# Kernel tuning notes

Measured on AMD Instinct MI355X. Metric: run time of the kernel, lower is better.

Reference implementation:

```python
import jax, jax.numpy as jnp
import numpy as np

B, H, T = 32, 80, 1600
C1, C2 = 32, 32
K, S, P = 3, 2, 1  # kernel, stride, padding on both dims


def setup_inputs() -> dict:
    key = jax.random.key(0)
    k1, k2, k3, k4, k5, k6 = jax.random.split(key, 6)
    inputs = jax.random.normal(k1, (B, 1, H, T), dtype=jnp.float32)
    seq_lengths = jax.random.randint(k2, (B,), 1, T + 1).astype(jnp.int32)
    W1 = jax.random.normal(k3, (C1, 1, K, K), dtype=jnp.float32) * 0.1
    b1 = jax.random.normal(k4, (C1,), dtype=jnp.float32) * 0.1
    W2 = jax.random.normal(k5, (C2, C1, K, K), dtype=jnp.float32) * 0.05
    b2 = jax.random.normal(k6, (C2,), dtype=jnp.float32) * 0.1
    return {"inputs": inputs, "seq_lengths": seq_lengths,
            "W1": W1, "b1": b1, "W2": W2, "b2": b2}


def _conv(x, W, b):
    y = jax.lax.conv_general_dilated(
        x, W, window_strides=(S, S), padding=((P, P), (P, P)),
        dimension_numbers=("NCHW", "OIHW", "NCHW"))
    return y + b[None, :, None, None]


def _new_lengths(L):
    # floor((L + 2p - d*(k-1) - 1)/s) + 1, matching _get_sequence_lengths
    return (L + 2 * P - (K - 1) - 1) // S + 1


def _mask_time(x, L):
    # zero positions t >= L[b] along the last (time) axis
    t = jnp.arange(x.shape[3])
    valid = (t[None, :] < L[:, None]).astype(x.dtype)  # [B, Tout]
    return x * valid[:, None, None, :]


def reference(inputs, seq_lengths, W1, b1, W2, b2):
    # conv1 + mask
    x = _conv(inputs, W1, b1)
    L = _new_lengths(seq_lengths)
    x = _mask_time(x, L)
    # relu + mask (lengths unchanged)
    x = _mask_time(jax.nn.relu(x), L)
    # conv2 + mask
    x = _conv(x, W2, b2)
    L = _new_lengths(L)
    x = _mask_time(x, L)
    # relu + mask
    x = _mask_time(jax.nn.relu(x), L)
    return x, L
```

## Files before the change

kernel.cpp:

```cpp
#include <hip/hip_runtime.h>
#include <hip/hip_bf16.h>

#define B_    32
#define H_IN  80
#define T_IN  1600
#define C1_   32
#define H1_   40
#define T1_   800
#define C2_   32
#define H2_   20
#define T2_   400

#define TH2   2
#define TT2   32
#define NH1   5
#define NT1   65
#define NIDX  33
#define RROWS 11
#define RCW   68
#define NX4   (RROWS * 34)

#define NPOS   (NH1 * NT1)
#define NCHUNK 11

#define WS_W2FRAGS 1152
#define WS_W1OFF   1152
#define WS_TOTAL   1216
#define OUTN  (B_ * C2_ * H2_ * T2_)

typedef unsigned int uint32;
typedef __attribute__((ext_vector_type(8)))  short short8;
typedef __attribute__((ext_vector_type(4)))  float f32x4;
typedef __attribute__((ext_vector_type(16))) float f32x16;
typedef __attribute__((ext_vector_type(2)))  uint32 u32x2;
typedef __attribute__((ext_vector_type(4)))  uint32 u32x4;

__device__ __forceinline__ unsigned short f2bf(float x) {
    __hip_bfloat16 h = __float2bfloat16(x);
    return __builtin_bit_cast(unsigned short, h);
}

__device__ __forceinline__ int x1off(int h1r, int t1r, int g) {
    int idx = t1r >> 1;
    int par = t1r & 1;
    return ((par * (NH1 * NIDX) + h1r * NIDX + idx) << 6) + (((g ^ idx) & 3) << 4);
}

__global__ void wprep(const float* __restrict__ W2, const float* __restrict__ W1,
                      const float* __restrict__ b1, unsigned short* __restrict__ ws) {
    int i = blockIdx.x * 256 + threadIdx.x;
    if (i < WS_W2FRAGS) {
        int mt   = i / 576;
        int rem  = i - mt * 576;
        int tap  = rem >> 6;
        int lane = rem & 63;
        int lg   = lane >> 4;
        int l15  = lane & 15;
        int c2   = mt * 16 + l15;
        short8 f;
#pragma unroll
        for (int j = 0; j < 8; ++j)
            f[j] = (short)f2bf(W2[((c2 * C1_) + lg * 8 + j) * 9 + tap]);
        *((short8*)ws + i) = f;
    } else if (i < WS_TOTAL) {
        int lane = i - WS_W1OFF;
        int c1 = lane & 31;
        int kb = (lane >> 5) * 8;
        short8 f;
#pragma unroll
        for (int j = 0; j < 8; ++j) {
            int k = kb + j;
            float v = (k < 9) ? W1[c1 * 9 + k] : (k == 9 ? b1[c1] : 0.0f);
            f[j] = (short)f2bf(v);
        }
        *((short8*)ws + i) = f;
    }
}

__global__ __launch_bounds__(256, 6) void fused_conv(
    const float* __restrict__ in, const int* __restrict__ seq,
    const float* __restrict__ b2,
    const unsigned short* __restrict__ ws,
    float* __restrict__ out)
{
    __shared__ __align__(16) char   x1mem[2 * NH1 * NIDX * 64];
    __shared__ __align__(16) uint32 raw32[RROWS * RCW];

    const int tid  = threadIdx.x;
    const int lane = tid & 63;
    const int wv   = tid >> 6;
    const int l15  = lane & 15;
    const int lg   = lane >> 4;
    const int hi   = lane >> 5;
    const int n32  = lane & 31;
    const int b      = blockIdx.z;
    const int h2base = blockIdx.y * TH2;
    const int t2base = blockIdx.x * TT2;

    const int L  = seq[b];
    const int L1 = ((L  - 1) >> 1) + 1;
    const int L2 = ((L1 - 1) >> 1) + 1;

    if (blockIdx.x == 0 && blockIdx.y == 0 && tid == 0)
        out[OUTN + b] = (float)L2;

    if (t2base >= L2) {
        const f32x4 z4 = (f32x4){0.f, 0.f, 0.f, 0.f};
#pragma unroll
        for (int k = 0; k < 2; ++k) {
            int i = tid + k * 256;
            int row = i >> 3, q = i & 7;
            int c2 = row >> 1, r = row & 1;
            int t2g = t2base + 4 * q;
            if (t2g < T2_)
                __builtin_nontemporal_store(z4,
                    (f32x4*)(out + ((b * C2_ + c2) * H2_ + h2base + r) * T2_ + t2g));
        }
        return;
    }

    const int row0 = 4 * h2base - 3;
    const int tA   = 4 * t2base - 4;
    const float* inb = in + b * (H_IN * T_IN);
#pragma unroll
    for (int k = 0; k < 2; ++k) {
        int it = tid + k * 256;
        if (it < NX4) {
            int row = it / 34;
            int j   = it - row * 34;
            int h = row0 + row;
            int t = tA + 4 * j;
            bool okq = (h >= 0) & (h < H_IN) & (t >= 0) & (t < T_IN);
            int basec = okq ? (h * T_IN + t) : 0;
            f32x4 v = *(const f32x4*)(inb + basec);
            float f0 = okq ? v[0] : 0.0f;
            float f1 = okq ? v[1] : 0.0f;
            float f2 = okq ? v[2] : 0.0f;
            float f3 = okq ? v[3] : 0.0f;
            u32x2 dw;
            dw.x = (uint32)f2bf(f0) | ((uint32)f2bf(f1) << 16);
            dw.y = (uint32)f2bf(f2) | ((uint32)f2bf(f3) << 16);
            *(u32x2*)(raw32 + row * RCW + 2 * j) = dw;
        }
    }

    const short8 w1f = *((const short8*)ws + WS_W1OFF + lane);
    const int mt    = wv & 1;
    const int strip = wv >> 1;
    short8 afr[9];
#pragma unroll
    for (int tap = 0; tap < 9; ++tap)
        afr[tap] = *((const short8*)ws + (mt * 9 + tap) * 64 + lane);
    float b2r[4];
#pragma unroll
    for (int j = 0; j < 4; ++j) b2r[j] = b2[mt * 16 + lg * 4 + j];

    __syncthreads();

    const int h1base = 2 * h2base - 1;
    const int t1base = 2 * t2base - 1;
    for (int c = wv; c < NCHUNK; c += 4) {
        int p  = c * 32 + n32;
        int pc = p < NPOS ? p : NPOS - 1;
        int h1r = pc / NT1;
        int t1r = pc - h1r * NT1;

        const uint32* rp = raw32 + (2 * h1r) * RCW + t1r;
        uint32 a0 = rp[0],          b0v = rp[1];
        uint32 a1 = rp[RCW],        b1v = rp[RCW + 1];
        uint32 a2 = rp[2 * RCW],    b2v = rp[2 * RCW + 1];

        uint32 w0l = (a0 >> 16) | (b0v << 16);
        uint32 w1l = (b0v >> 16) | (a1 & 0xffff0000u);
        uint32 w2l = b1v;
        uint32 w3l = (a2 >> 16) | (b2v << 16);
        uint32 w0h = (b2v >> 16) | 0x3f800000u;

        uint32 fw0 = hi ? w0h : w0l;
        uint32 fw1 = hi ? 0u  : w1l;
        uint32 fw2 = hi ? 0u  : w2l;
        uint32 fw3 = hi ? 0u  : w3l;
        short8 bfrag = __builtin_bit_cast(short8, (u32x4){fw0, fw1, fw2, fw3});

        f32x16 acc = {};
        acc = __builtin_amdgcn_mfma_f32_32x32x16_bf16(w1f, bfrag, acc, 0, 0, 0);

        int h1 = h1base + h1r;
        int t1 = t1base + t1r;
        bool okp = (h1 >= 0) && (t1 >= 0) && (t1 < L1);
        if (p < NPOS) {
#pragma unroll
            for (int g = 0; g < 4; ++g) {
                float v0 = okp ? fmaxf(acc[4 * g + 0], 0.0f) : 0.0f;
                float v1 = okp ? fmaxf(acc[4 * g + 1], 0.0f) : 0.0f;
                float v2 = okp ? fmaxf(acc[4 * g + 2], 0.0f) : 0.0f;
                float v3 = okp ? fmaxf(acc[4 * g + 3], 0.0f) : 0.0f;
                u32x2 dw;
                dw.x = (uint32)f2bf(v0) | ((uint32)f2bf(v1) << 16);
                dw.y = (uint32)f2bf(v2) | ((uint32)f2bf(v3) << 16);
                *(u32x2*)(x1mem + x1off(h1r, t1r, g) + hi * 8) = dw;
            }
        }
    }

    __syncthreads();

    f32x4 acc2[TH2];
#pragma unroll
    for (int r = 0; r < TH2; ++r) acc2[r] = (f32x4){0.f, 0.f, 0.f, 0.f};

#pragma unroll
    for (int tap = 0; tap < 9; ++tap) {
        const int kh = tap / 3;
        const int kt = tap % 3;
        const int t1r = 2 * (strip * 16 + l15) + kt;
#pragma unroll
        for (int r = 0; r < TH2; ++r) {
            short8 bx = *(const short8*)(x1mem + x1off(2 * r + kh, t1r, lg));
            acc2[r] = __builtin_amdgcn_mfma_f32_16x16x32_bf16(afr[tap], bx, acc2[r], 0, 0, 0);
        }
    }

    {
        const int t2 = t2base + strip * 16 + l15;
        const bool vm = (t2 < L2);
        if (t2 < T2_) {
            float* outb = out + ((b * C2_) * H2_ + h2base) * T2_ + t2;
#pragma unroll
            for (int r = 0; r < TH2; ++r) {
#pragma unroll
                for (int j = 0; j < 4; ++j) {
                    int c2 = mt * 16 + lg * 4 + j;
                    float v = acc2[r][j] + b2r[j];
                    v = vm ? fmaxf(v, 0.0f) : 0.0f;
                    __builtin_nontemporal_store(v, outb + (c2 * H2_ + r) * T2_);
                }
            }
        }
    }
}

extern "C" void kernel_launch(void* const* d_in, const int* in_sizes, int n_in,
                              void* d_out, int out_size, void* d_ws, size_t ws_size,
                              hipStream_t stream) {
    const float* in  = (const float*)d_in[0];
    const int*   seq = (const int*)d_in[1];
    const float* W1  = (const float*)d_in[2];
    const float* b1  = (const float*)d_in[3];
    const float* W2  = (const float*)d_in[4];
    const float* b2  = (const float*)d_in[5];
    float* out = (float*)d_out;
    unsigned short* ws = (unsigned short*)d_ws;

    wprep<<<dim3((WS_TOTAL + 255) / 256), dim3(256), 0, stream>>>(W2, W1, b1, ws);

    dim3 grid((T2_ + TT2 - 1) / TT2, H2_ / TH2, B_);
    fused_conv<<<grid, dim3(256), 0, stream>>>(in, seq, b2, ws, out);
}
```

Measured before the change: 22.27 us.

## Make fused conv persistent with atomic tile scheduler and register-prefetched input

```diff
diff --git a/kernel.cpp b/kernel.cpp
--- a/kernel.cpp
+++ b/kernel.cpp
@@ -23,9 +23,15 @@
 #define NPOS   (NH1 * NT1)
 #define NCHUNK 11
 
+#define NT2I   13
+#define NH2I   10
+#define NTILES (NT2I * NH2I * B_)
+#define NBLK   1536
+
 #define WS_W2FRAGS 1152
 #define WS_W1OFF   1152
 #define WS_TOTAL   1216
+#define CTR_OFF    (WS_TOTAL * 16)
 #define OUTN  (B_ * C2_ * H2_ * T2_)
 
 typedef unsigned int uint32;
@@ -49,6 +55,7 @@
 __global__ void wprep(const float* __restrict__ W2, const float* __restrict__ W1,
                       const float* __restrict__ b1, unsigned short* __restrict__ ws) {
     int i = blockIdx.x * 256 + threadIdx.x;
+    if (i == 0) *(uint32*)((char*)ws + CTR_OFF) = 0u;
     if (i < WS_W2FRAGS) {
         int mt   = i / 576;
         int rem  = i - mt * 576;
@@ -77,14 +84,41 @@
     }
 }
 
+__device__ __forceinline__ void stage_to_regs(const float* __restrict__ inb, int tid,
+                                              int h2base, int t2base, u32x2 dw[2]) {
+    const int row0 = 4 * h2base - 3;
+    const int tA   = 4 * t2base - 4;
+#pragma unroll
+    for (int k = 0; k < 2; ++k) {
+        int it = tid + k * 256;
+        u32x2 d = (u32x2){0u, 0u};
+        if (it < NX4) {
+            int row = it / 34;
+            int j   = it - row * 34;
+            int h = row0 + row;
+            int t = tA + 4 * j;
+            bool okq = (h >= 0) & (h < H_IN) & (t >= 0) & (t < T_IN);
+            f32x4 v = *(const f32x4*)(inb + (okq ? h * T_IN + t : 0));
+            float f0 = okq ? v[0] : 0.0f;
+            float f1 = okq ? v[1] : 0.0f;
+            float f2 = okq ? v[2] : 0.0f;
+            float f3 = okq ? v[3] : 0.0f;
+            d.x = (uint32)f2bf(f0) | ((uint32)f2bf(f1) << 16);
+            d.y = (uint32)f2bf(f2) | ((uint32)f2bf(f3) << 16);
+        }
+        dw[k] = d;
+    }
+}
+
 __global__ __launch_bounds__(256, 6) void fused_conv(
     const float* __restrict__ in, const int* __restrict__ seq,
     const float* __restrict__ b2,
-    const unsigned short* __restrict__ ws,
+    unsigned short* __restrict__ ws,
     float* __restrict__ out)
 {
     __shared__ __align__(16) char   x1mem[2 * NH1 * NIDX * 64];
     __shared__ __align__(16) uint32 raw32[RROWS * RCW];
+    __shared__ int s_tile[2];
 
     const int tid  = threadIdx.x;
     const int lane = tid & 63;
@@ -93,56 +127,8 @@
     const int lg   = lane >> 4;
     const int hi   = lane >> 5;
     const int n32  = lane & 31;
-    const int b      = blockIdx.z;
-    const int h2base = blockIdx.y * TH2;
-    const int t2base = blockIdx.x * TT2;
-
-    const int L  = seq[b];
-    const int L1 = ((L  - 1) >> 1) + 1;
-    const int L2 = ((L1 - 1) >> 1) + 1;
-
-    if (blockIdx.x == 0 && blockIdx.y == 0 && tid == 0)
-        out[OUTN + b] = (float)L2;
-
-    if (t2base >= L2) {
-        const f32x4 z4 = (f32x4){0.f, 0.f, 0.f, 0.f};
-#pragma unroll
-        for (int k = 0; k < 2; ++k) {
-            int i = tid + k * 256;
-            int row = i >> 3, q = i & 7;
-            int c2 = row >> 1, r = row & 1;
-            int t2g = t2base + 4 * q;
-            if (t2g < T2_)
-                __builtin_nontemporal_store(z4,
-                    (f32x4*)(out + ((b * C2_ + c2) * H2_ + h2base + r) * T2_ + t2g));
-        }
-        return;
-    }
-
-    const int row0 = 4 * h2base - 3;
-    const int tA   = 4 * t2base - 4;
-    const float* inb = in + b * (H_IN * T_IN);
-#pragma unroll
-    for (int k = 0; k < 2; ++k) {
-        int it = tid + k * 256;
-        if (it < NX4) {
-            int row = it / 34;
-            int j   = it - row * 34;
-            int h = row0 + row;
-            int t = tA + 4 * j;
-            bool okq = (h >= 0) & (h < H_IN) & (t >= 0) & (t < T_IN);
-            int basec = okq ? (h * T_IN + t) : 0;
-            f32x4 v = *(const f32x4*)(inb + basec);
-            float f0 = okq ? v[0] : 0.0f;
-            float f1 = okq ? v[1] : 0.0f;
-            float f2 = okq ? v[2] : 0.0f;
-            float f3 = okq ? v[3] : 0.0f;
-            u32x2 dw;
-            dw.x = (uint32)f2bf(f0) | ((uint32)f2bf(f1) << 16);
-            dw.y = (uint32)f2bf(f2) | ((uint32)f2bf(f3) << 16);
-            *(u32x2*)(raw32 + row * RCW + 2 * j) = dw;
-        }
-    }
+
+    uint32* counter = (uint32*)((char*)ws + CTR_OFF);
 
     const short8 w1f = *((const short8*)ws + WS_W1OFF + lane);
     const int mt    = wv & 1;
@@ -155,88 +141,158 @@
 #pragma unroll
     for (int j = 0; j < 4; ++j) b2r[j] = b2[mt * 16 + lg * 4 + j];
 
+    if (tid == 0) s_tile[0] = (int)atomicAdd(counter, 1u);
     __syncthreads();
-
-    const int h1base = 2 * h2base - 1;
-    const int t1base = 2 * t2base - 1;
-    for (int c = wv; c < NCHUNK; c += 4) {
-        int p  = c * 32 + n32;
-        int pc = p < NPOS ? p : NPOS - 1;
-        int h1r = pc / NT1;
-        int t1r = pc - h1r * NT1;
-
-        const uint32* rp = raw32 + (2 * h1r) * RCW + t1r;
-        uint32 a0 = rp[0],          b0v = rp[1];
-        uint32 a1 = rp[RCW],        b1v = rp[RCW + 1];
-        uint32 a2 = rp[2 * RCW],    b2v = rp[2 * RCW + 1];
-
-        uint32 w0l = (a0 >> 16) | (b0v << 16);
-        uint32 w1l = (b0v >> 16) | (a1 & 0xffff0000u);
-        uint32 w2l = b1v;
-        uint32 w3l = (a2 >> 16) | (b2v << 16);
-        uint32 w0h = (b2v >> 16) | 0x3f800000u;
-
-        uint32 fw0 = hi ? w0h : w0l;
-        uint32 fw1 = hi ? 0u  : w1l;
-        uint32 fw2 = hi ? 0u  : w2l;
-        uint32 fw3 = hi ? 0u  : w3l;
-        short8 bfrag = __builtin_bit_cast(short8, (u32x4){fw0, fw1, fw2, fw3});
-
-        f32x16 acc = {};
-        acc = __builtin_amdgcn_mfma_f32_32x32x16_bf16(w1f, bfrag, acc, 0, 0, 0);
-
-        int h1 = h1base + h1r;
-        int t1 = t1base + t1r;
-        bool okp = (h1 >= 0) && (t1 >= 0) && (t1 < L1);
-        if (p < NPOS) {
-#pragma unroll
-            for (int g = 0; g < 4; ++g) {
-                float v0 = okp ? fmaxf(acc[4 * g + 0], 0.0f) : 0.0f;
-                float v1 = okp ? fmaxf(acc[4 * g + 1], 0.0f) : 0.0f;
-                float v2 = okp ? fmaxf(acc[4 * g + 2], 0.0f) : 0.0f;
-                float v3 = okp ? fmaxf(acc[4 * g + 3], 0.0f) : 0.0f;
-                u32x2 dw;
-                dw.x = (uint32)f2bf(v0) | ((uint32)f2bf(v1) << 16);
-                dw.y = (uint32)f2bf(v2) | ((uint32)f2bf(v3) << 16);
-                *(u32x2*)(x1mem + x1off(h1r, t1r, g) + hi * 8) = dw;
-            }
-        }
+    int tile = s_tile[0];
+
+    int b = 0, h2base = 0, t2base = 0, L1 = 0, L2 = 0;
+    bool work = false;
+    u32x2 dw[2];
+    if (tile < NTILES) {
+        b = tile / (NT2I * NH2I);
+        int rem = tile - b * (NT2I * NH2I);
+        h2base = (rem / NT2I) * TH2;
+        t2base = (rem % NT2I) * TT2;
+        int L = seq[b];
+        L1 = ((L - 1) >> 1) + 1;
+        L2 = ((L1 - 1) >> 1) + 1;
+        work = (t2base < L2);
+        if (work) stage_to_regs(in + b * (H_IN * T_IN), tid, h2base, t2base, dw);
     }
 
-    __syncthreads();
-
-    f32x4 acc2[TH2];
-#pragma unroll
-    for (int r = 0; r < TH2; ++r) acc2[r] = (f32x4){0.f, 0.f, 0.f, 0.f};
-
-#pragma unroll
-    for (int tap = 0; tap < 9; ++tap) {
-        const int kh = tap / 3;
-        const int kt = tap % 3;
-        const int t1r = 2 * (strip * 16 + l15) + kt;
-#pragma unroll
-        for (int r = 0; r < TH2; ++r) {
-            short8 bx = *(const short8*)(x1mem + x1off(2 * r + kh, t1r, lg));
-            acc2[r] = __builtin_amdgcn_mfma_f32_16x16x32_bf16(afr[tap], bx, acc2[r], 0, 0, 0);
-        }
-    }
-
-    {
-        const int t2 = t2base + strip * 16 + l15;
-        const bool vm = (t2 < L2);
-        if (t2 < T2_) {
-            float* outb = out + ((b * C2_) * H2_ + h2base) * T2_ + t2;
-#pragma unroll
-            for (int r = 0; r < TH2; ++r) {
-#pragma unroll
-                for (int j = 0; j < 4; ++j) {
-                    int c2 = mt * 16 + lg * 4 + j;
-                    float v = acc2[r][j] + b2r[j];
-                    v = vm ? fmaxf(v, 0.0f) : 0.0f;
-                    __builtin_nontemporal_store(v, outb + (c2 * H2_ + r) * T2_);
+    int p = 0;
+    while (tile < NTILES) {
+        if (tid == 0 && (t2base == 0) && (h2base == 0))
+            out[OUTN + b] = (float)L2;
+
+        if (work) {
+#pragma unroll
+            for (int k = 0; k < 2; ++k) {
+                int it = tid + k * 256;
+                if (it < NX4) {
+                    int row = it / 34;
+                    int j   = it - row * 34;
+                    *(u32x2*)(raw32 + row * RCW + 2 * j) = dw[k];
                 }
             }
         }
+
+        if (tid == 0) s_tile[p ^ 1] = (int)atomicAdd(counter, 1u);
+        __syncthreads();
+        const int next = s_tile[p ^ 1];
+
+        int nb = 0, nh2 = 0, nt2 = 0, nL1 = 0, nL2 = 0;
+        bool nwork = false;
+        u32x2 ndw[2];
+        if (next < NTILES) {
+            nb = next / (NT2I * NH2I);
+            int rem = next - nb * (NT2I * NH2I);
+            nh2 = (rem / NT2I) * TH2;
+            nt2 = (rem % NT2I) * TT2;
+            int L = seq[nb];
+            nL1 = ((L - 1) >> 1) + 1;
+            nL2 = ((nL1 - 1) >> 1) + 1;
+            nwork = (nt2 < nL2);
+            if (nwork) stage_to_regs(in + nb * (H_IN * T_IN), tid, nh2, nt2, ndw);
+        }
+
+        if (work) {
+            const int h1base = 2 * h2base - 1;
+            const int t1base = 2 * t2base - 1;
+            for (int c = wv; c < NCHUNK; c += 4) {
+                int pp = c * 32 + n32;
+                int pc = pp < NPOS ? pp : NPOS - 1;
+                int h1r = pc / NT1;
+                int t1r = pc - h1r * NT1;
+
+                const uint32* rp = raw32 + (2 * h1r) * RCW + t1r;
+                uint32 a0 = rp[0],          b0v = rp[1];
+                uint32 a1 = rp[RCW],        b1v = rp[RCW + 1];
+                uint32 a2 = rp[2 * RCW],    b2v = rp[2 * RCW + 1];
+
+                uint32 w0l = (a0 >> 16) | (b0v << 16);
+                uint32 w1l = (b0v >> 16) | (a1 & 0xffff0000u);
+                uint32 w2l = b1v;
+                uint32 w3l = (a2 >> 16) | (b2v << 16);
+                uint32 w0h = (b2v >> 16) | 0x3f800000u;
+
+                uint32 fw0 = hi ? w0h : w0l;
+                uint32 fw1 = hi ? 0u  : w1l;
+                uint32 fw2 = hi ? 0u  : w2l;
+                uint32 fw3 = hi ? 0u  : w3l;
+                short8 bfrag = __builtin_bit_cast(short8, (u32x4){fw0, fw1, fw2, fw3});
+
+                f32x16 acc = {};
+                acc = __builtin_amdgcn_mfma_f32_32x32x16_bf16(w1f, bfrag, acc, 0, 0, 0);
+
+                int h1 = h1base + h1r;
+                int t1 = t1base + t1r;
+                bool okp = (h1 >= 0) && (t1 >= 0) && (t1 < L1);
+                if (pp < NPOS) {
+#pragma unroll
+                    for (int g = 0; g < 4; ++g) {
+                        float v0 = okp ? fmaxf(acc[4 * g + 0], 0.0f) : 0.0f;
+                        float v1 = okp ? fmaxf(acc[4 * g + 1], 0.0f) : 0.0f;
+                        float v2 = okp ? fmaxf(acc[4 * g + 2], 0.0f) : 0.0f;
+                        float v3 = okp ? fmaxf(acc[4 * g + 3], 0.0f) : 0.0f;
+                        u32x2 dd;
+                        dd.x = (uint32)f2bf(v0) | ((uint32)f2bf(v1) << 16);
+                        dd.y = (uint32)f2bf(v2) | ((uint32)f2bf(v3) << 16);
+                        *(u32x2*)(x1mem + x1off(h1r, t1r, g) + hi * 8) = dd;
+                    }
+                }
+            }
+            __syncthreads();
+
+            f32x4 acc2[TH2];
+#pragma unroll
+            for (int r = 0; r < TH2; ++r) acc2[r] = (f32x4){0.f, 0.f, 0.f, 0.f};
+#pragma unroll
+            for (int tap = 0; tap < 9; ++tap) {
+                const int kh = tap / 3;
+                const int kt = tap % 3;
+                const int t1r = 2 * (strip * 16 + l15) + kt;
+#pragma unroll
+                for (int r = 0; r < TH2; ++r) {
+                    short8 bx = *(const short8*)(x1mem + x1off(2 * r + kh, t1r, lg));
+                    acc2[r] = __builtin_amdgcn_mfma_f32_16x16x32_bf16(afr[tap], bx, acc2[r], 0, 0, 0);
+                }
+            }
+            {
+                const int t2 = t2base + strip * 16 + l15;
+                const bool vm = (t2 < L2);
+                if (t2 < T2_) {
+                    float* outb = out + ((b * C2_) * H2_ + h2base) * T2_ + t2;
+#pragma unroll
+                    for (int r = 0; r < TH2; ++r) {
+#pragma unroll
+                        for (int j = 0; j < 4; ++j) {
+                            int c2 = mt * 16 + lg * 4 + j;
+                            float v = acc2[r][j] + b2r[j];
+                            v = vm ? fmaxf(v, 0.0f) : 0.0f;
+                            __builtin_nontemporal_store(v, outb + (c2 * H2_ + r) * T2_);
+                        }
+                    }
+                }
+            }
+        } else {
+            const f32x4 z4 = (f32x4){0.f, 0.f, 0.f, 0.f};
+#pragma unroll
+            for (int k = 0; k < 2; ++k) {
+                int i = tid + k * 256;
+                int row = i >> 3, q = i & 7;
+                int c2 = row >> 1, r = row & 1;
+                int t2g = t2base + 4 * q;
+                if (t2g < T2_)
+                    __builtin_nontemporal_store(z4,
+                        (f32x4*)(out + ((b * C2_ + c2) * H2_ + h2base + r) * T2_ + t2g));
+            }
+        }
+
+        tile = next;
+        b = nb; h2base = nh2; t2base = nt2; L1 = nL1; L2 = nL2; work = nwork;
+        dw[0] = ndw[0]; dw[1] = ndw[1];
+        p ^= 1;
     }
 }
 
@@ -254,6 +310,5 @@
 
     wprep<<<dim3((WS_TOTAL + 255) / 256), dim3(256), 0, stream>>>(W2, W1, b1, ws);
 
-    dim3 grid((T2_ + TT2 - 1) / TT2, H2_ / TH2, B_);
-    fused_conv<<<grid, dim3(256), 0, stream>>>(in, seq, b2, ws, out);
-}
+    fused_conv<<<dim3(NBLK), dim3(256), 0, stream>>>(in, seq, b2, ws, out);
+}
```

Result: slower. 83.00 us (+272.7%).
